# Performance work log

Hardware: AMD Instinct MI355X
Metric: run time of the kernel (lower is better)

Reference implementation:

```python
import jax, jax.numpy as jnp
import numpy as np

N = 100000      # nodes
E = 1000000     # edges per directional view
D = 128         # feature dim (all layers)
NG, OG = 4, 32  # n_gram_len, one_gram_dim (NG*OG == D)
L = 2           # conv layers (layer_dims=[128,128,128])
DEC = 64        # decoder hidden = D // 2
CLS = 64        # task classes
L2_EPS = 1e-12


def setup_inputs() -> dict:
    key = jax.random.key(0)
    ks = iter(jax.random.split(key, 40))
    nrm = lambda shape, s=0.05: jax.random.normal(next(ks), shape, dtype=jnp.float32) * s
    inp = {
        'x': jax.random.normal(next(ks), (N, D), dtype=jnp.float32),
        'edge_index_in': jax.random.randint(next(ks), (2, E), 0, N, dtype=jnp.int32),
        'edge_weight_in': jax.random.uniform(next(ks), (E,), dtype=jnp.float32),
        'edge_index_out': jax.random.randint(next(ks), (2, E), 0, N, dtype=jnp.int32),
        'edge_weight_out': jax.random.uniform(next(ks), (E,), dtype=jnp.float32),
        'edge_index_und': jax.random.randint(next(ks), (2, E), 0, N, dtype=jnp.int32),
        'edge_weight_und': jax.random.uniform(next(ks), (E,), dtype=jnp.float32),
        'pe': nrm((NG, OG)),
        # per-layer stacked params (both layers are D->D)
        'W_main_in': nrm((L, D, D)),
        'W_main_out': nrm((L, D, D)),
        'W_shared': nrm((L, D, D)),
        'W_und': nrm((L, D, D)),
        'b_main_in': nrm((L, D), 0.01),
        'b_main_out': nrm((L, D), 0.01),
        'b_shared_in': nrm((L, D), 0.01),
        'b_shared_out': nrm((L, D), 0.01),
        'b_und': nrm((L, D), 0.01),
        'C_in_vec': jnp.ones((L, N, 1), jnp.float32) + nrm((L, N, 1), 0.01),
        'C_out_vec': jnp.ones((L, N, 1), jnp.float32) + nrm((L, N, 1), 0.01),
        'C_all_vec': jnp.ones((L, N, 1), jnp.float32) + nrm((L, N, 1), 0.01),
        'constant': nrm((L, N, D)),
        'Wd1': nrm((DEC, D)),
        'bd1': nrm((DEC,), 0.01),
        'Wd2': nrm((CLS, DEC)),
        'bd2': nrm((CLS,), 0.01),
    }
    return inp


def reference(x, edge_index_in, edge_weight_in, edge_index_out, edge_weight_out,
              edge_index_und, edge_weight_und, pe,
              W_main_in, W_main_out, W_shared, W_und,
              b_main_in, b_main_out, b_shared_in, b_shared_out, b_und,
              C_in_vec, C_out_vec, C_all_vec, constant,
              Wd1, bd1, Wd2, bd2):
    n = x.shape[0]

    def prop(ei, ew, h):
        # message: edge_weight * x_j (gather from src=ei[0]); aggr='add' at dst=ei[1]
        msg = ew[:, None] * h[ei[0]]                      # [E, D]
        return jax.ops.segment_sum(msg, ei[1], num_segments=n)

    # positional encoding over n-gram sub-blocks
    h = (x.reshape(n, NG, OG) + pe[None]).reshape(n, NG * OG)

    for i in range(L):
        h_res = h
        hs = h @ W_shared[i].T                            # shared transform (computed once)
        ic = (prop(edge_index_in, edge_weight_in, h @ W_main_in[i].T) + b_main_in[i]
              + prop(edge_index_in, edge_weight_in, hs) + b_shared_in[i])
        oc = (prop(edge_index_out, edge_weight_out, h @ W_main_out[i].T) + b_main_out[i]
              + prop(edge_index_out, edge_weight_out, hs) + b_shared_out[i])
        ac = prop(edge_index_und, edge_weight_und, h @ W_und[i].T) + b_und[i]
        gcn = C_all_vec[i] * ac + C_in_vec[i] * ic + C_out_vec[i] * oc + constant[i]
        # res_proj is Identity (in_dim == out_dim); dropout inactive (eval)
        h = jax.nn.leaky_relu(gcn + h_res)

    z = jax.nn.relu(h @ Wd1.T + bd1)
    logits = z @ Wd2.T + bd2
    logp = jax.nn.log_softmax(logits, axis=-1)
    emb = h / jnp.maximum(jnp.linalg.norm(h, axis=-1, keepdims=True), L2_EPS)
    return (logp, emb)
```

## Files before the change

kernel.cpp:

```cpp
#include <hip/hip_runtime.h>
#include <math.h>

#define NN 100000
#define EE 1000000
#define DD 128
#define CLS 64

#define NB 196
#define CHUNK 4096
#define NCH 245
#define SLOTS (3 * NB * NCH)
#define CAPB 8192

typedef short bf16x8 __attribute__((ext_vector_type(8)));
typedef float f32x4 __attribute__((ext_vector_type(4)));

static __device__ __forceinline__ short f2bf(float f) {
  union { float f; unsigned u; } v; v.f = f;
  unsigned r = v.u + 0x7FFF + ((v.u >> 16) & 1);
  return (short)(r >> 16);
}
static __device__ __forceinline__ unsigned pack2(float a, float b) {
  return ((unsigned)(unsigned short)f2bf(b) << 16) | (unsigned short)f2bf(a);
}
static __device__ __forceinline__ float bf_lo(unsigned u) {
  union { unsigned u; float f; } v; v.u = u << 16; return v.f;
}
static __device__ __forceinline__ float bf_hi(unsigned u) {
  union { unsigned u; float f; } v; v.u = u & 0xffff0000u; return v.f;
}
static __device__ __forceinline__ float bfs(short s) {
  union { unsigned u; float f; } v; v.u = ((unsigned)(unsigned short)s) << 16; return v.f;
}

__global__ __launch_bounds__(256) void pe_kernel(const float* __restrict__ x,
                                                 const float* __restrict__ pe,
                                                 short* __restrict__ h) {
  int idx8 = blockIdx.x * 256 + threadIdx.x;
  int d0 = (idx8 & 15) * 8;
  float4 a = *(const float4*)&x[(size_t)idx8 * 8];
  float4 b = *(const float4*)&x[(size_t)idx8 * 8 + 4];
  float4 pa = *(const float4*)&pe[d0];
  float4 pb = *(const float4*)&pe[d0 + 4];
  int4 o;
  o.x = pack2(a.x + pa.x, a.y + pa.y);
  o.y = pack2(a.z + pa.z, a.w + pa.w);
  o.z = pack2(b.x + pb.x, b.y + pb.y);
  o.w = pack2(b.z + pb.z, b.w + pb.w);
  *(int4*)&h[(size_t)idx8 * 8] = o;
}

__global__ __launch_bounds__(256) void wprep_kernel(const float* __restrict__ Wmi,
                                                    const float* __restrict__ Wmo,
                                                    const float* __restrict__ Wsh,
                                                    const float* __restrict__ Wu,
                                                    short* __restrict__ Wcat) {
  int idx = blockIdx.x * 256 + threadIdx.x;
  int l = idx / 49152;
  int r = idx - l * 49152;
  int j = r >> 7, k = r & 127;
  float v;
  if (j < 128)      v = Wmi[l*16384 + j*128 + k] + Wsh[l*16384 + j*128 + k];
  else if (j < 256) v = Wmo[l*16384 + (j-128)*128 + k] + Wsh[l*16384 + (j-128)*128 + k];
  else              v = Wu[l*16384 + (j-256)*128 + k];
  Wcat[idx] = f2bf(v);
}

__global__ __launch_bounds__(256) void countA_kernel(const int* __restrict__ ei0,
                                                     const int* __restrict__ ei1,
                                                     const int* __restrict__ ei2,
                                                     int* __restrict__ counts) {
  __shared__ int c[NB];
  int v = blockIdx.y, ch = blockIdx.x, tid = threadIdx.x;
  const int* dstp = ((v == 0) ? ei0 : (v == 1) ? ei1 : ei2) + EE;
  for (int i = tid; i < NB; i += 256) c[i] = 0;
  __syncthreads();
  int s = ch * CHUNK, e = (s + CHUNK < EE) ? s + CHUNK : EE;
  for (int i = s + tid; i < e; i += 256) atomicAdd(&c[dstp[i] >> 9], 1);
  __syncthreads();
  for (int b = tid; b < NB; b += 256) counts[(v * NB + b) * NCH + ch] = c[b];
}

__global__ __launch_bounds__(256) void scan1_kernel(const int* __restrict__ counts,
                                                    int* __restrict__ S,
                                                    int* __restrict__ bsums, int n) {
  __shared__ int sd[256];
  int t = threadIdx.x;
  int base = blockIdx.x * 1024 + t * 4;
  int4 v = make_int4(0, 0, 0, 0);
  if (base + 3 < n) {
    v = *(const int4*)&counts[base];
  } else {
    if (base + 0 < n) v.x = counts[base + 0];
    if (base + 1 < n) v.y = counts[base + 1];
    if (base + 2 < n) v.z = counts[base + 2];
    if (base + 3 < n) v.w = counts[base + 3];
  }
  int ts = v.x + v.y + v.z + v.w;
  sd[t] = ts;
  __syncthreads();
  for (int off = 1; off < 256; off <<= 1) {
    int xel = (t >= off) ? sd[t - off] : 0;
    __syncthreads();
    sd[t] += xel;
    __syncthreads();
  }
  int excl = sd[t] - ts;
  int o0 = excl, o1 = o0 + v.x, o2 = o1 + v.y, o3 = o2 + v.z;
  if (base + 0 < n) S[base + 0] = o0;
  if (base + 1 < n) S[base + 1] = o1;
  if (base + 2 < n) S[base + 2] = o2;
  if (base + 3 < n) S[base + 3] = o3;
  if (t == 255) bsums[blockIdx.x] = sd[255];
}

__global__ void scan2_kernel(int* __restrict__ bsums, int nb) {
  __shared__ int sd[512];
  int t = threadIdx.x;
  int v = (t < nb) ? bsums[t] : 0;
  sd[t] = v;
  __syncthreads();
  for (int off = 1; off < 512; off <<= 1) {
    int xel = (t >= off) ? sd[t - off] : 0;
    __syncthreads();
    sd[t] += xel;
    __syncthreads();
  }
  if (t < nb) bsums[t] = sd[t] - v;
}

__global__ __launch_bounds__(256) void scan3_kernel(int* __restrict__ S,
                                                    const int* __restrict__ bsums, int n) {
  int i = blockIdx.x * 256 + threadIdx.x;
  if (i < n) S[i] += bsums[i >> 10];
}

__global__ __launch_bounds__(256) void partA_kernel(const int* __restrict__ ei0,
                                                    const int* __restrict__ ei1,
                                                    const int* __restrict__ ei2,
                                                    const float* __restrict__ ew0,
                                                    const float* __restrict__ ew1,
                                                    const float* __restrict__ ew2,
                                                    const int* __restrict__ S,
                                                    int2* __restrict__ binned) {
  __shared__ int cur[NB];
  int v = blockIdx.y, ch = blockIdx.x, tid = threadIdx.x;
  const int* ei = (v == 0) ? ei0 : (v == 1) ? ei1 : ei2;
  const float* ew = (v == 0) ? ew0 : (v == 1) ? ew1 : ew2;
  for (int b = tid; b < NB; b += 256) cur[b] = S[(v * NB + b) * NCH + ch];
  __syncthreads();
  int s = ch * CHUNK, e = (s + CHUNK < EE) ? s + CHUNK : EE;
  for (int i = s + tid; i < e; i += 256) {
    int src = ei[i];
    int dst = ei[EE + i];
    float w = ew[i];
    int b = dst >> 9;
    int pos = atomicAdd(&cur[b], 1);
    binned[pos] = make_int2(src | ((dst & 511) << 17), __float_as_int(w));
  }
}

__global__ __launch_bounds__(256) void buildB_kernel(const int2* __restrict__ binned,
                                                     const int* __restrict__ S,
                                                     unsigned* __restrict__ csr4,
                                                     int* __restrict__ offs) {
  __shared__ int2 recs[CAPB];
  __shared__ int cnt[512];
  __shared__ int pref[512];
  __shared__ int sd[256];
  int gb = blockIdx.x, tid = threadIdx.x;
  int v = gb / NB, b = gb - v * NB;
  int base = S[gb * NCH];
  int next = (gb == 3 * NB - 1) ? 3 * EE : S[(gb + 1) * NCH];
  int n = next - base;
  for (int i = tid; i < 512; i += 256) cnt[i] = 0;
  int m = n < CAPB ? n : CAPB;
  for (int i = tid; i < m; i += 256) recs[i] = binned[base + i];
  __syncthreads();
  for (int i = tid; i < n; i += 256) {
    int2 r = (i < CAPB) ? recs[i] : binned[base + i];
    atomicAdd(&cnt[(r.x >> 17) & 511], 1);
  }
  __syncthreads();
  int c0 = cnt[2 * tid], c1 = cnt[2 * tid + 1];
  int ssum = c0 + c1;
  sd[tid] = ssum;
  __syncthreads();
  for (int off = 1; off < 256; off <<= 1) {
    int x = (tid >= off) ? sd[tid - off] : 0;
    __syncthreads();
    sd[tid] += x;
    __syncthreads();
  }
  int excl = sd[tid] - ssum;
  pref[2 * tid] = excl;
  pref[2 * tid + 1] = excl + c0;
  __syncthreads();
  int node0 = b * 512;
  for (int i = tid; i < 512; i += 256) {
    int node = node0 + i;
    if (node < NN) offs[v * NN + node] = base + pref[i];
  }
  if (gb == 0 && tid == 0) offs[3 * NN] = 3 * EE;
  for (int i = tid; i < 512; i += 256) cnt[i] = pref[i];
  __syncthreads();
  for (int i = tid; i < n; i += 256) {
    int2 r = (i < CAPB) ? recs[i] : binned[base + i];
    int nl = (r.x >> 17) & 511;
    int p = atomicAdd(&cnt[nl], 1);
    float w = __int_as_float(r.y);
    unsigned wb = (unsigned)(unsigned short)f2bf(w);
    csr4[base + p] = (wb << 17) | (unsigned)(r.x & 0x1FFFF);
  }
}

__global__ __launch_bounds__(256) void agg3_kernel(
    const short* __restrict__ h, const unsigned* __restrict__ csr4,
    const int* __restrict__ offs, short* __restrict__ g) {
  int gid = blockIdx.x * 256 + threadIdx.x;
  int v = gid >> 6;
  int lane = gid & 63;
  int f0 = lane * 2;

#pragma unroll
  for (int view = 0; view < 3; ++view) {
    int s = offs[view * NN + v];
    int e = offs[view * NN + v + 1];
    float accx = 0.f, accy = 0.f;
    for (int base = s; base < e; base += 64) {
      int cnt = e - base; if (cnt > 64) cnt = 64;
      int r = 0;
      if (lane < cnt) r = (int)csr4[base + lane];
      int j = 0;
      for (; j + 3 < cnt; j += 4) {
        unsigned r0 = (unsigned)__shfl(r, j);
        unsigned r1 = (unsigned)__shfl(r, j + 1);
        unsigned r2 = (unsigned)__shfl(r, j + 2);
        unsigned r3 = (unsigned)__shfl(r, j + 3);
        float w0 = __uint_as_float((r0 >> 17) << 16);
        float w1 = __uint_as_float((r1 >> 17) << 16);
        float w2 = __uint_as_float((r2 >> 17) << 16);
        float w3 = __uint_as_float((r3 >> 17) << 16);
        unsigned u0 = *(const unsigned*)&h[(size_t)(r0 & 0x1FFFF) * 128 + f0];
        unsigned u1 = *(const unsigned*)&h[(size_t)(r1 & 0x1FFFF) * 128 + f0];
        unsigned u2 = *(const unsigned*)&h[(size_t)(r2 & 0x1FFFF) * 128 + f0];
        unsigned u3 = *(const unsigned*)&h[(size_t)(r3 & 0x1FFFF) * 128 + f0];
        accx += w0 * bf_lo(u0) + w1 * bf_lo(u1) + w2 * bf_lo(u2) + w3 * bf_lo(u3);
        accy += w0 * bf_hi(u0) + w1 * bf_hi(u1) + w2 * bf_hi(u2) + w3 * bf_hi(u3);
      }
      for (; j < cnt; ++j) {
        unsigned r0 = (unsigned)__shfl(r, j);
        float w0 = __uint_as_float((r0 >> 17) << 16);
        unsigned u0 = *(const unsigned*)&h[(size_t)(r0 & 0x1FFFF) * 128 + f0];
        accx += w0 * bf_lo(u0);
        accy += w0 * bf_hi(u0);
      }
    }
    *(unsigned*)&g[(size_t)view * ((size_t)NN * 128) + (size_t)v * 128 + f0] =
        pack2(accx, accy);
  }
}

#define LW 136
__global__ __launch_bounds__(256) void mmc_kernel(
    const short* __restrict__ g, const short* __restrict__ WcatL,
    const float* __restrict__ b_mi, const float* __restrict__ b_mo,
    const float* __restrict__ b_si, const float* __restrict__ b_so,
    const float* __restrict__ b_u,
    const float* __restrict__ Cin, const float* __restrict__ Cou,
    const float* __restrict__ Cal,
    const float* __restrict__ cst, const short* __restrict__ h_prev,
    short* __restrict__ h_out) {
  __shared__ short As[128 * LW];
  __shared__ short Bs[128 * LW];
  __shared__ float cvs[3][128];
  __shared__ float bias[3][128];
  int tid = threadIdx.x;
  int rowbase = blockIdx.x * 128;

  if (tid < 128) {
    int r = tid;
    int gr = rowbase + r; if (gr >= NN) gr = NN - 1;
    cvs[0][r] = Cin[gr];
    cvs[1][r] = Cou[gr];
    cvs[2][r] = Cal[gr];
  } else {
    int c = tid - 128;
    bias[0][c] = b_mi[c] + b_si[c];
    bias[1][c] = b_mo[c] + b_so[c];
    bias[2][c] = b_u[c];
  }

  int w = tid >> 6, lane = tid & 63;
  int wr = (w >> 1) * 64, wc = (w & 1) * 64;
  int lrow = lane & 15, quad = lane >> 4;

  f32x4 comb[4][4];
#pragma unroll
  for (int mi = 0; mi < 4; ++mi)
#pragma unroll
    for (int ni = 0; ni < 4; ++ni) comb[mi][ni] = (f32x4){0.f, 0.f, 0.f, 0.f};

  for (int view = 0; view < 3; ++view) {
    __syncthreads();
    const short* gv = g + (size_t)view * ((size_t)NN * 128);
    for (int idx = tid; idx < 2048; idx += 256) {
      int r = idx >> 4, c8 = (idx & 15) * 8;
      int gr = rowbase + r; if (gr >= NN) gr = NN - 1;
      float cv = cvs[view][r];
      int4 u = *(const int4*)&gv[(size_t)gr * 128 + c8];
      int4 o;
      o.x = pack2(cv * bf_lo((unsigned)u.x), cv * bf_hi((unsigned)u.x));
      o.y = pack2(cv * bf_lo((unsigned)u.y), cv * bf_hi((unsigned)u.y));
      o.z = pack2(cv * bf_lo((unsigned)u.z), cv * bf_hi((unsigned)u.z));
      o.w = pack2(cv * bf_lo((unsigned)u.w), cv * bf_hi((unsigned)u.w));
      *(int4*)&As[r * LW + c8] = o;
      *(int4*)&Bs[r * LW + c8] = *(const int4*)&WcatL[(view * 128 + r) * 128 + c8];
    }
    __syncthreads();

#pragma unroll
    for (int k0 = 0; k0 < 128; k0 += 32) {
      bf16x8 a[4], b[4];
#pragma unroll
      for (int mi = 0; mi < 4; ++mi)
        a[mi] = *(const bf16x8*)&As[(wr + mi * 16 + lrow) * LW + k0 + quad * 8];
#pragma unroll
      for (int ni = 0; ni < 4; ++ni)
        b[ni] = *(const bf16x8*)&Bs[(wc + ni * 16 + lrow) * LW + k0 + quad * 8];
#pragma unroll
      for (int mi = 0; mi < 4; ++mi)
#pragma unroll
        for (int ni = 0; ni < 4; ++ni)
          comb[mi][ni] = __builtin_amdgcn_mfma_f32_16x16x32_bf16(a[mi], b[ni], comb[mi][ni], 0, 0, 0);
    }
  }

  __syncthreads();
#pragma unroll
  for (int mi = 0; mi < 4; ++mi) {
#pragma unroll
    for (int r = 0; r < 4; ++r) {
      int rl = wr + mi * 16 + quad * 4 + r;
      int row = rowbase + rl;
      int grow = (row < NN) ? row : NN - 1;
      float ci = cvs[0][rl], co = cvs[1][rl], ca = cvs[2][rl];
#pragma unroll
      for (int ni = 0; ni < 4; ++ni) {
        int cl = wc + ni * 16 + lrow;
        float val = comb[mi][ni][r]
                  + ci * bias[0][cl] + co * bias[1][cl] + ca * bias[2][cl]
                  + cst[(size_t)grow * 128 + cl]
                  + bfs(h_prev[(size_t)grow * 128 + cl]);
        val = val > 0.f ? val : 0.01f * val;
        Bs[rl * LW + cl] = f2bf(val);
      }
    }
  }
  __syncthreads();

  for (int idx = tid; idx < 2048; idx += 256) {
    int r = idx >> 4, c8 = (idx & 15) * 8;
    int row = rowbase + r;
    if (row < NN)
      *(int4*)&h_out[(size_t)row * 128 + c8] = *(const int4*)&Bs[r * LW + c8];
  }
}

__global__ __launch_bounds__(256) void dec_kernel(const short* __restrict__ h,
                                                  const float* __restrict__ Wd1,
                                                  const float* __restrict__ bd1,
                                                  const float* __restrict__ Wd2,
                                                  const float* __restrict__ bd2,
                                                  float* __restrict__ out_logp,
                                                  float* __restrict__ out_emb) {
  __shared__ float Hs[32 * 128];
  __shared__ float W1t[64 * 66];
  __shared__ float W2t[64 * 66];
  __shared__ float Zs[32 * 68];
  int tid = threadIdx.x;
  int base = blockIdx.x * 32;

  for (int idx = tid; idx < 2048; idx += 256) {
    unsigned u = *(const unsigned*)&h[(size_t)base * 128 + idx * 2];
    Hs[idx * 2] = bf_lo(u);
    Hs[idx * 2 + 1] = bf_hi(u);
  }
  for (int idx = tid; idx < 4096; idx += 256) {
    int c = idx >> 6, k = idx & 63;
    W2t[k * 66 + c] = Wd2[idx];
  }

  int j = tid & 63;
  int rg = tid >> 6;
  float zacc[8];
#pragma unroll
  for (int r = 0; r < 8; ++r) zacc[r] = 0.f;

  for (int kk = 0; kk < 128; kk += 64) {
    __syncthreads();
    for (int idx = tid; idx < 4096; idx += 256) {
      int jj = idx >> 6, k = idx & 63;
      W1t[k * 66 + jj] = Wd1[jj * 128 + kk + k];
    }
    __syncthreads();
    for (int k = 0; k < 64; ++k) {
      float w = W1t[k * 66 + j];
#pragma unroll
      for (int r = 0; r < 8; ++r) zacc[r] += Hs[(rg * 8 + r) * 128 + kk + k] * w;
    }
  }
  float b1 = bd1[j];
#pragma unroll
  for (int r = 0; r < 8; ++r) {
    float z = zacc[r] + b1;
    Zs[(rg * 8 + r) * 68 + j] = z > 0.f ? z : 0.f;
  }
  __syncthreads();

  float b2 = bd2[j];
  float lg[8];
#pragma unroll
  for (int i = 0; i < 8; ++i) lg[i] = b2;
  for (int k = 0; k < 64; ++k) {
    float w = W2t[k * 66 + j];
#pragma unroll
    for (int i = 0; i < 8; ++i) lg[i] += Zs[(rg + 4 * i) * 68 + k] * w;
  }

#pragma unroll
  for (int i = 0; i < 8; ++i) {
    float m = lg[i];
    for (int d = 1; d < 64; d <<= 1) m = fmaxf(m, __shfl_xor(m, d));
    float s = expf(lg[i] - m);
    for (int d = 1; d < 64; d <<= 1) s += __shfl_xor(s, d);
    float lp = lg[i] - m - logf(s);
    out_logp[(size_t)(base + rg + 4 * i) * 64 + j] = lp;
  }

#pragma unroll
  for (int i = 0; i < 8; ++i) {
    int r = rg + 4 * i;
    float v1 = Hs[r * 128 + j];
    float v2 = Hs[r * 128 + 64 + j];
    float ss = v1 * v1 + v2 * v2;
    for (int d = 1; d < 64; d <<= 1) ss += __shfl_xor(ss, d);
    float nrm = sqrtf(ss);
    float sc = 1.f / fmaxf(nrm, 1e-12f);
    size_t o = (size_t)(base + r) * 128;
    out_emb[o + j] = v1 * sc;
    out_emb[o + 64 + j] = v2 * sc;
  }
}

extern "C" void kernel_launch(void* const* d_in, const int* in_sizes, int n_in,
                              void* d_out, int out_size, void* d_ws, size_t ws_size,
                              hipStream_t stream) {
  const float* x   = (const float*)d_in[0];
  const int* eiI   = (const int*)d_in[1];
  const float* ewI = (const float*)d_in[2];
  const int* eiO   = (const int*)d_in[3];
  const float* ewO = (const float*)d_in[4];
  const int* eiU   = (const int*)d_in[5];
  const float* ewU = (const float*)d_in[6];
  const float* pe  = (const float*)d_in[7];
  const float* Wmi = (const float*)d_in[8];
  const float* Wmo = (const float*)d_in[9];
  const float* Wsh = (const float*)d_in[10];
  const float* Wu  = (const float*)d_in[11];
  const float* bmi = (const float*)d_in[12];
  const float* bmo = (const float*)d_in[13];
  const float* bsi = (const float*)d_in[14];
  const float* bso = (const float*)d_in[15];
  const float* bu  = (const float*)d_in[16];
  const float* Cin = (const float*)d_in[17];
  const float* Cou = (const float*)d_in[18];
  const float* Cal = (const float*)d_in[19];
  const float* cst = (const float*)d_in[20];
  const float* Wd1 = (const float*)d_in[21];
  const float* bd1 = (const float*)d_in[22];
  const float* Wd2 = (const float*)d_in[23];
  const float* bd2 = (const float*)d_in[24];

  const size_t ND = (size_t)NN * DD;
  short* wsS = (short*)d_ws;
  short* hA   = wsS;
  short* hB   = hA + ND;
  short* g    = hB + ND;
  short* Wcat = g + 3 * ND;
  int2* binned   = (int2*)(Wcat + 98304);
  unsigned* csr4 = (unsigned*)(binned + (size_t)3 * EE);
  int* S      = (int*)(csr4 + (size_t)3 * EE);
  int* bsums  = S + SLOTS + 4;
  int* offs   = bsums + 512;

  pe_kernel<<<6250, 256, 0, stream>>>(x, pe, hA);
  wprep_kernel<<<384, 256, 0, stream>>>(Wmi, Wmo, Wsh, Wu, Wcat);

  dim3 chGrid(NCH, 3);
  countA_kernel<<<chGrid, 256, 0, stream>>>(eiI, eiO, eiU, S);
  const int nb1 = (SLOTS + 1023) / 1024;
  scan1_kernel<<<nb1, 256, 0, stream>>>(S, S, bsums, SLOTS);
  scan2_kernel<<<1, 512, 0, stream>>>(bsums, nb1);
  scan3_kernel<<<(SLOTS + 255) / 256, 256, 0, stream>>>(S, bsums, SLOTS);
  partA_kernel<<<chGrid, 256, 0, stream>>>(eiI, eiO, eiU, ewI, ewO, ewU, S, binned);
  buildB_kernel<<<3 * NB, 256, 0, stream>>>(binned, S, csr4, offs);

  const short* hin = hA;
  short* hout = hB;
  dim3 mmGrid((NN + 127) / 128);
  for (int l = 0; l < 2; ++l) {
    agg3_kernel<<<25000, 256, 0, stream>>>(hin, csr4, offs, g);
    mmc_kernel<<<mmGrid, 256, 0, stream>>>(g, Wcat + l * 49152,
                                           bmi + l * DD, bmo + l * DD,
                                           bsi + l * DD, bso + l * DD, bu + l * DD,
                                           Cin + l * NN, Cou + l * NN, Cal + l * NN,
                                           cst + (size_t)l * ND, hin, hout);
    short* tmp = (short*)hin;
    hin = hout;
    hout = tmp;
  }

  float* out_logp = (float*)d_out;
  float* out_emb = out_logp + (size_t)NN * CLS;
  dec_kernel<<<3125, 256, 0, stream>>>(hin, Wd1, bd1, Wd2, bd2, out_logp, out_emb);
}
```

Measured before the change: 821.0 us.

## Rewrite decoder kernel to use bf16 MFMA with 128-row tiles

Replaces the scalar FP32 decoder matmuls with bf16 MFMA 16x16x32 instructions. Each block now handles 128 rows instead of 32, and the weights are converted to bf16 in shared memory. The hidden activation z is rounded to bf16 before the second matmul. The logits are staged through reused shared memory for the log-softmax. This cuts ALU time in the decoder but adds precision loss from bf16 weights and z.

```diff
diff --git a/kernel.cpp b/kernel.cpp
--- a/kernel.cpp
+++ b/kernel.cpp
@@ -367,6 +367,7 @@
   }
 }
 
+#define ZW 72
 __global__ __launch_bounds__(256) void dec_kernel(const short* __restrict__ h,
                                                   const float* __restrict__ Wd1,
                                                   const float* __restrict__ bd1,
@@ -374,82 +375,142 @@
                                                   const float* __restrict__ bd2,
                                                   float* __restrict__ out_logp,
                                                   float* __restrict__ out_emb) {
-  __shared__ float Hs[32 * 128];
-  __shared__ float W1t[64 * 66];
-  __shared__ float W2t[64 * 66];
-  __shared__ float Zs[32 * 68];
+  __shared__ short As[128 * LW];
+  __shared__ short B1s[64 * LW];
+  __shared__ short Zs[128 * ZW];
+  __shared__ short B2s[64 * ZW];
+  float* Ls = (float*)As;
+
   int tid = threadIdx.x;
-  int base = blockIdx.x * 32;
+  int rowbase = blockIdx.x * 128;
 
   for (int idx = tid; idx < 2048; idx += 256) {
-    unsigned u = *(const unsigned*)&h[(size_t)base * 128 + idx * 2];
-    Hs[idx * 2] = bf_lo(u);
-    Hs[idx * 2 + 1] = bf_hi(u);
-  }
-  for (int idx = tid; idx < 4096; idx += 256) {
-    int c = idx >> 6, k = idx & 63;
-    W2t[k * 66 + c] = Wd2[idx];
-  }
-
-  int j = tid & 63;
-  int rg = tid >> 6;
-  float zacc[8];
-#pragma unroll
-  for (int r = 0; r < 8; ++r) zacc[r] = 0.f;
-
-  for (int kk = 0; kk < 128; kk += 64) {
-    __syncthreads();
-    for (int idx = tid; idx < 4096; idx += 256) {
-      int jj = idx >> 6, k = idx & 63;
-      W1t[k * 66 + jj] = Wd1[jj * 128 + kk + k];
-    }
-    __syncthreads();
-    for (int k = 0; k < 64; ++k) {
-      float w = W1t[k * 66 + j];
-#pragma unroll
-      for (int r = 0; r < 8; ++r) zacc[r] += Hs[(rg * 8 + r) * 128 + kk + k] * w;
-    }
-  }
-  float b1 = bd1[j];
-#pragma unroll
-  for (int r = 0; r < 8; ++r) {
-    float z = zacc[r] + b1;
-    Zs[(rg * 8 + r) * 68 + j] = z > 0.f ? z : 0.f;
-  }
-  __syncthreads();
-
-  float b2 = bd2[j];
-  float lg[8];
-#pragma unroll
-  for (int i = 0; i < 8; ++i) lg[i] = b2;
-  for (int k = 0; k < 64; ++k) {
-    float w = W2t[k * 66 + j];
-#pragma unroll
-    for (int i = 0; i < 8; ++i) lg[i] += Zs[(rg + 4 * i) * 68 + k] * w;
-  }
-
-#pragma unroll
-  for (int i = 0; i < 8; ++i) {
-    float m = lg[i];
-    for (int d = 1; d < 64; d <<= 1) m = fmaxf(m, __shfl_xor(m, d));
-    float s = expf(lg[i] - m);
-    for (int d = 1; d < 64; d <<= 1) s += __shfl_xor(s, d);
-    float lp = lg[i] - m - logf(s);
-    out_logp[(size_t)(base + rg + 4 * i) * 64 + j] = lp;
-  }
-
-#pragma unroll
-  for (int i = 0; i < 8; ++i) {
+    int r = idx >> 4, c8 = (idx & 15) * 8;
+    int gr = rowbase + r; if (gr >= NN) gr = NN - 1;
+    *(int4*)&As[r * LW + c8] = *(const int4*)&h[(size_t)gr * 128 + c8];
+  }
+  for (int idx = tid; idx < 2048; idx += 256) {
+    int j = idx >> 5, k4 = (idx & 31) * 4;
+    float4 wv = *(const float4*)&Wd1[j * 128 + k4];
+    uint2 o; o.x = pack2(wv.x, wv.y); o.y = pack2(wv.z, wv.w);
+    *(uint2*)&B1s[j * LW + k4] = o;
+  }
+  for (int idx = tid; idx < 1024; idx += 256) {
+    int j = idx >> 4, k4 = (idx & 15) * 4;
+    float4 wv = *(const float4*)&Wd2[j * 64 + k4];
+    uint2 o; o.x = pack2(wv.x, wv.y); o.y = pack2(wv.z, wv.w);
+    *(uint2*)&B2s[j * ZW + k4] = o;
+  }
+  __syncthreads();
+
+  int w = tid >> 6, lane = tid & 63;
+  int wr = w * 32;
+  int lrow = lane & 15, quad = lane >> 4;
+
+  float b1c[4], b2c[4];
+#pragma unroll
+  for (int ni = 0; ni < 4; ++ni) {
+    b1c[ni] = bd1[ni * 16 + lrow];
+    b2c[ni] = bd2[ni * 16 + lrow];
+  }
+
+  f32x4 acc1[2][4];
+#pragma unroll
+  for (int mi = 0; mi < 2; ++mi)
+#pragma unroll
+    for (int ni = 0; ni < 4; ++ni) acc1[mi][ni] = (f32x4){0.f, 0.f, 0.f, 0.f};
+#pragma unroll
+  for (int k0 = 0; k0 < 128; k0 += 32) {
+    bf16x8 a[2], b[4];
+#pragma unroll
+    for (int mi = 0; mi < 2; ++mi)
+      a[mi] = *(const bf16x8*)&As[(wr + mi * 16 + lrow) * LW + k0 + quad * 8];
+#pragma unroll
+    for (int ni = 0; ni < 4; ++ni)
+      b[ni] = *(const bf16x8*)&B1s[(ni * 16 + lrow) * LW + k0 + quad * 8];
+#pragma unroll
+    for (int mi = 0; mi < 2; ++mi)
+#pragma unroll
+      for (int ni = 0; ni < 4; ++ni)
+        acc1[mi][ni] = __builtin_amdgcn_mfma_f32_16x16x32_bf16(a[mi], b[ni], acc1[mi][ni], 0, 0, 0);
+  }
+#pragma unroll
+  for (int mi = 0; mi < 2; ++mi)
+#pragma unroll
+    for (int ni = 0; ni < 4; ++ni)
+#pragma unroll
+      for (int r = 0; r < 4; ++r) {
+        int rl = wr + mi * 16 + quad * 4 + r;
+        int cl = ni * 16 + lrow;
+        float z = acc1[mi][ni][r] + b1c[ni];
+        Zs[rl * ZW + cl] = f2bf(z > 0.f ? z : 0.f);
+      }
+  __syncthreads();
+
+  f32x4 acc2[2][4];
+#pragma unroll
+  for (int mi = 0; mi < 2; ++mi)
+#pragma unroll
+    for (int ni = 0; ni < 4; ++ni) acc2[mi][ni] = (f32x4){0.f, 0.f, 0.f, 0.f};
+#pragma unroll
+  for (int k0 = 0; k0 < 64; k0 += 32) {
+    bf16x8 a[2], b[4];
+#pragma unroll
+    for (int mi = 0; mi < 2; ++mi)
+      a[mi] = *(const bf16x8*)&Zs[(wr + mi * 16 + lrow) * ZW + k0 + quad * 8];
+#pragma unroll
+    for (int ni = 0; ni < 4; ++ni)
+      b[ni] = *(const bf16x8*)&B2s[(ni * 16 + lrow) * ZW + k0 + quad * 8];
+#pragma unroll
+    for (int mi = 0; mi < 2; ++mi)
+#pragma unroll
+      for (int ni = 0; ni < 4; ++ni)
+        acc2[mi][ni] = __builtin_amdgcn_mfma_f32_16x16x32_bf16(a[mi], b[ni], acc2[mi][ni], 0, 0, 0);
+  }
+
+  int j = lane;
+  int rg = w;
+#pragma unroll
+  for (int i = 0; i < 32; ++i) {
     int r = rg + 4 * i;
-    float v1 = Hs[r * 128 + j];
-    float v2 = Hs[r * 128 + 64 + j];
+    float v1 = bfs(As[r * LW + j]);
+    float v2 = bfs(As[r * LW + 64 + j]);
     float ss = v1 * v1 + v2 * v2;
     for (int d = 1; d < 64; d <<= 1) ss += __shfl_xor(ss, d);
     float nrm = sqrtf(ss);
     float sc = 1.f / fmaxf(nrm, 1e-12f);
-    size_t o = (size_t)(base + r) * 128;
-    out_emb[o + j] = v1 * sc;
-    out_emb[o + 64 + j] = v2 * sc;
+    int row = rowbase + r;
+    if (row < NN) {
+      size_t o = (size_t)row * 128;
+      out_emb[o + j] = v1 * sc;
+      out_emb[o + 64 + j] = v2 * sc;
+    }
+  }
+  __syncthreads();
+
+#pragma unroll
+  for (int mi = 0; mi < 2; ++mi)
+#pragma unroll
+    for (int ni = 0; ni < 4; ++ni)
+#pragma unroll
+      for (int r = 0; r < 4; ++r) {
+        int rl = wr + mi * 16 + quad * 4 + r;
+        int cl = ni * 16 + lrow;
+        Ls[rl * 68 + cl] = acc2[mi][ni][r] + b2c[ni];
+      }
+  __syncthreads();
+
+#pragma unroll
+  for (int i = 0; i < 32; ++i) {
+    int r = rg + 4 * i;
+    float lg = Ls[r * 68 + j];
+    float m = lg;
+    for (int d = 1; d < 64; d <<= 1) m = fmaxf(m, __shfl_xor(m, d));
+    float s = expf(lg - m);
+    for (int d = 1; d < 64; d <<= 1) s += __shfl_xor(s, d);
+    float lp = lg - m - logf(s);
+    int row = rowbase + r;
+    if (row < NN) out_logp[(size_t)row * 64 + j] = lp;
   }
 }
 
@@ -523,5 +584,5 @@
 
   float* out_logp = (float*)d_out;
   float* out_emb = out_logp + (size_t)NN * CLS;
-  dec_kernel<<<3125, 256, 0, stream>>>(hin, Wd1, bd1, Wd2, bd2, out_logp, out_emb);
-}
+  dec_kernel<<<mmGrid, 256, 0, stream>>>(hin, Wd1, bd1, Wd2, bd2, out_logp, out_emb);
+}
```

New measurement: 764.4 us. 1.07x faster.
